# Optimization experiments

Hardware: AMD Instinct MI355X
Metric: run time of the kernel (lower is better)

The kernel has to match this reference:

```python
import jax, jax.numpy as jnp
import numpy as np

INPUT_DIM = 1024
HIDDEN = 64
NUM_MEM = 8   # +1 shared slot -> 9 total
K = 2
SEQ = 256
BATCH = 32


def setup_inputs() -> dict:
    key = jax.random.key(0)
    ks = jax.random.split(key, 10)
    s = 1.0 / np.sqrt(INPUT_DIM)
    nm1 = NUM_MEM + 1
    return {
        "X": jax.random.normal(ks[0], (SEQ, BATCH, INPUT_DIM), jnp.float32),
        "M_0": jnp.zeros((BATCH, nm1, HIDDEN, HIDDEN), jnp.float32),
        "Wk_w": jax.random.uniform(ks[1], (HIDDEN * nm1, INPUT_DIM), jnp.float32, -s, s),
        "Wk_b": jax.random.uniform(ks[2], (HIDDEN * nm1,), jnp.float32, -s, s),
        "Wv_w": jax.random.uniform(ks[3], (HIDDEN * nm1, INPUT_DIM), jnp.float32, -s, s),
        "Wv_b": jax.random.uniform(ks[4], (HIDDEN * nm1,), jnp.float32, -s, s),
        "Wg_w": jax.random.uniform(ks[5], (NUM_MEM, INPUT_DIM), jnp.float32, -s, s),
        "Wg_b": jax.random.uniform(ks[6], (NUM_MEM,), jnp.float32, -s, s),
        "Wq_w": jax.random.uniform(ks[7], (HIDDEN, INPUT_DIM), jnp.float32, -s, s),
        "Wq_b": jax.random.uniform(ks[8], (HIDDEN,), jnp.float32, -s, s),
    }


def _mom_forward(X, M_0, Wk_w, Wk_b, Wv_w, Wv_b, Wg_w, Wg_b, Wq_w, Wq_b):
    B = X.shape[1]
    nm1 = NUM_MEM + 1
    b_idx = jnp.arange(B)[:, None]

    def step(M, x_t):
        # gating + top-k routing (sorted descending, like torch.topk)
        score = jax.nn.softmax(x_t @ Wg_w.T + Wg_b, axis=1)          # (B, NUM_MEM)
        m_scores, m_idx = jax.lax.top_k(score, K)                    # (B, K)
        idx_update = jnp.concatenate(
            [jnp.zeros((B, 1), jnp.int32), m_idx.astype(jnp.int32)], axis=1)  # (B, K+1)
        g = m_scores / jnp.sum(m_scores, axis=1, keepdims=True)     # (B, K)

        Mk = (x_t @ Wk_w.T + Wk_b).reshape(B, nm1, HIDDEN)          # (B, 9, H)
        Mv = (x_t @ Wv_w.T + Wv_b).reshape(B, nm1, HIDDEN)
        # only gather the K+1 routed outer products instead of all 9
        k_sel = jnp.take_along_axis(Mk, idx_update[:, :, None], axis=1)  # (B, K+1, H)
        v_sel = jnp.take_along_axis(Mv, idx_update[:, :, None], axis=1)
        src = k_sel[..., :, None] * v_sel[..., None, :]              # (B, K+1, H, H)
        M = M.at[b_idx, idx_update].add(src)                         # scatter-add (dupes accumulate)

        M_use = M[b_idx, m_idx]                                      # (B, K, H, H)
        M_out = jnp.einsum('bk,bkij->bij', g, M_use) + M[:, 0]       # add shared memory
        q = x_t @ Wq_w.T + Wq_b                                      # (B, H)
        o = jnp.einsum('bi,bij->bj', q, M_out)                       # (B, H)
        return M, o

    M_final, outputs = jax.lax.scan(step, M_0, X)
    return outputs, M_final


def reference(X, M_0, Wk_w, Wk_b, Wv_w, Wv_b, Wg_w, Wg_b, Wq_w, Wq_b):
    return _mom_forward(X, M_0, Wk_w, Wk_b, Wv_w, Wv_b, Wg_w, Wg_b, Wq_w, Wq_b)
```

## Files before the change

### kernel.cpp

```cpp
#include <hip/hip_runtime.h>
#include <stdint.h>

#define SEQ 256
#define BATCH 32
#define IN_DIM 1024
#define HID 64
#define NPAD 1280
#define ROWS (SEQ*BATCH)

#define XBF_OFF   0
#define DMH_OFF   0
#define WBF_OFF   16777216
#define BB_OFF    19398656
#define GATE_OFF  19403776
#define Y_OFF     19534848

#define NC 8
#define CHL 32

#define DM_CB_U32 18432

typedef __attribute__((ext_vector_type(8))) short short8;
typedef __attribute__((ext_vector_type(4))) float floatx4;

typedef const __attribute__((address_space(1))) unsigned int gas_u32;
typedef __attribute__((address_space(3))) unsigned int las_u32;
static __device__ __forceinline__ void gl_lds16(const void* g, void* l) {
  __builtin_amdgcn_global_load_lds((gas_u32*)g, (las_u32*)l, 16, 0, 0);
}

static __device__ __forceinline__ short f2bf(float f) {
  union { float f; uint32_t u; } a; a.f = f;
  uint32_t r = (a.u + 0x7FFFu + ((a.u >> 16) & 1u)) >> 16;
  return (short)r;
}
static __device__ __forceinline__ float bflo(uint32_t u){ return __uint_as_float(u << 16); }
static __device__ __forceinline__ float bfhi(uint32_t u){ return __uint_as_float(u & 0xffff0000u); }
static __device__ __forceinline__ float bfu(unsigned short us){ return __uint_as_float(((uint32_t)us) << 16); }

__global__ __launch_bounds__(256) void prep_gate_kernel(
    const float* __restrict__ X,
    const float* __restrict__ Wk, const float* __restrict__ bk,
    const float* __restrict__ Wv, const float* __restrict__ bv,
    const float* __restrict__ Wg, const float* __restrict__ bg,
    const float* __restrict__ Wq, const float* __restrict__ bq,
    short* __restrict__ Xbf, short* __restrict__ Wbf,
    float* __restrict__ bb, float4* __restrict__ gate)
{
  if (blockIdx.x < 2048) {
    const int lane = threadIdx.x & 63;
    const int row  = blockIdx.x * 4 + (threadIdx.x >> 6);
    const float* x = X + (int64_t)row * IN_DIM;
    short4* xb = (short4*)(Xbf + (int64_t)row * IN_DIM);

    float acc[8];
#pragma unroll
    for (int e = 0; e < 8; e++) acc[e] = 0.f;
#pragma unroll
    for (int i = 0; i < 4; i++) {
      const int off = i * 256 + lane * 4;
      float4 xv = *(const float4*)(x + off);
      short4 s4;
      s4.x = f2bf(xv.x); s4.y = f2bf(xv.y); s4.z = f2bf(xv.z); s4.w = f2bf(xv.w);
      xb[i * 64 + lane] = s4;
#pragma unroll
      for (int e = 0; e < 8; e++) {
        float4 wv = *(const float4*)(Wg + e * IN_DIM + off);
        acc[e] += xv.x * wv.x + xv.y * wv.y + xv.z * wv.z + xv.w * wv.w;
      }
    }
#pragma unroll
    for (int e = 0; e < 8; e++) {
#pragma unroll
      for (int m = 32; m >= 1; m >>= 1)
        acc[e] += __shfl_xor(acc[e], m);
      acc[e] += bg[e];
    }
    if (lane == 0) {
      int i0 = 0; float v0 = acc[0];
#pragma unroll
      for (int e = 1; e < 8; e++) if (acc[e] > v0) { v0 = acc[e]; i0 = e; }
      int i1 = -1; float v1 = -3.4e38f;
#pragma unroll
      for (int e = 0; e < 8; e++) if (e != i0 && acc[e] > v1) { v1 = acc[e]; i1 = e; }
      float e1 = __expf(v1 - v0);
      float inv = 1.f / (1.f + e1);
      gate[row] = make_float4(__int_as_float(i0), __int_as_float(i1), inv, e1 * inv);
    }
  } else {
    const int idx = (blockIdx.x - 2048) * 256 + threadIdx.x;
    const int NW4 = NPAD * IN_DIM / 4;
#pragma unroll
    for (int i = idx; i < NW4; i += 65536) {
      int e = i * 4;
      int r = e >> 10;
      int k = e & 1023;
      float4 x;
      if (r < 576)       x = *(const float4*)(Wk + (int64_t)r*1024 + k);
      else if (r < 1152) x = *(const float4*)(Wv + (int64_t)(r-576)*1024 + k);
      else if (r < 1216) x = *(const float4*)(Wq + (int64_t)(r-1152)*1024 + k);
      else               x = make_float4(0.f, 0.f, 0.f, 0.f);
      short4 s4;
      s4.x = f2bf(x.x); s4.y = f2bf(x.y); s4.z = f2bf(x.z); s4.w = f2bf(x.w);
      ((short4*)Wbf)[i] = s4;
    }
    if (idx < NPAD) {
      int r = idx; float v;
      if (r < 576)       v = bk[r];
      else if (r < 1152) v = bv[r - 576];
      else if (r < 1216) v = bq[r - 1152];
      else               v = 0.f;
      bb[r] = v;
    }
  }
}

__global__ __launch_bounds__(256) void gemm_kernel(
    const short* __restrict__ Xbf,
    const short* __restrict__ Wbf,
    const float* __restrict__ bb,
    float* __restrict__ Y)
{
  __shared__ short As[128 * 32];
  __shared__ short Bs[128 * 32];

  const int tid  = threadIdx.x;
  const int lane = tid & 63;
  const int wv   = tid >> 6;
  const int quad = lane >> 4;
  const int cl   = lane & 15;
  const int wm   = wv & 1;
  const int wn   = wv >> 1;
  const int m0 = blockIdx.y * 128;
  const int n0 = blockIdx.x * 128;

  const int srow = wv * 32 + (lane >> 2);
  const int scol = (lane & 3) * 8;
  const short* gA = Xbf + (int64_t)(m0 + srow) * IN_DIM + scol;
  const short* gB = Wbf + (int64_t)(n0 + srow) * IN_DIM + scol;
  short* lA = As + (wv * 32) * 32;
  short* lB = Bs + (wv * 32) * 32;

  floatx4 acc[4][4];
#pragma unroll
  for (int i = 0; i < 4; i++)
#pragma unroll
    for (int k = 0; k < 4; k++) acc[i][k] = (floatx4){0.f, 0.f, 0.f, 0.f};

  for (int ks = 0; ks < IN_DIM; ks += 32) {
    gl_lds16(gA + ks,                lA);
    gl_lds16(gA + 16 * IN_DIM + ks,  lA + 16 * 32);
    gl_lds16(gB + ks,                lB);
    gl_lds16(gB + 16 * IN_DIM + ks,  lB + 16 * 32);
    __syncthreads();

    short8 bfrag[4], afrag[4];
#pragma unroll
    for (int nt = 0; nt < 4; nt++)
      bfrag[nt] = *(const short8*)(&Bs[(wn * 64 + nt * 16 + cl) * 32 + quad * 8]);
#pragma unroll
    for (int mt = 0; mt < 4; mt++)
      afrag[mt] = *(const short8*)(&As[(wm * 64 + mt * 16 + cl) * 32 + quad * 8]);
#pragma unroll
    for (int mt = 0; mt < 4; mt++)
#pragma unroll
      for (int nt = 0; nt < 4; nt++)
        acc[mt][nt] = __builtin_amdgcn_mfma_f32_16x16x32_bf16(afrag[mt], bfrag[nt], acc[mt][nt], 0, 0, 0);
    __syncthreads();
  }

#pragma unroll
  for (int nt = 0; nt < 4; nt++) {
    const int col = n0 + wn * 64 + nt * 16 + cl;
    const float bias = bb[col];
#pragma unroll
    for (int mt = 0; mt < 4; mt++) {
#pragma unroll
      for (int r = 0; r < 4; r++) {
        int row = m0 + wm * 64 + mt * 16 + quad * 4 + r;
        Y[(int64_t)row * NPAD + col] = acc[mt][nt][r] + bias;
      }
    }
  }
}

__global__ __launch_bounds__(512) void mfma_chunk_kernel(
    const float* __restrict__ Y, const float4* __restrict__ gate,
    unsigned short* __restrict__ DMu, float* __restrict__ out)
{
  __shared__ uint32_t Qs[32 * 32];
  __shared__ uint32_t Ks[96 * 32];
  __shared__ unsigned short Kts[64 * 104];
  __shared__ unsigned short Vts[64 * 104];
  __shared__ unsigned short Ps[32 * 104];
  __shared__ float4 gl[32];
  __shared__ uint32_t su[96];

  const int blk = blockIdx.x;
  const int c   = blk & 7;
  const int b   = blk >> 3;
  const int tid = threadIdx.x;
  const int lane = tid & 63;
  const int wv  = tid >> 6;
  const int quad = lane >> 4;
  const int cl  = lane & 15;
  const int t0  = c * CHL;

  if (tid < 32) {
    float4 g = gate[(t0 + tid) * BATCH + b];
    gl[tid] = g;
    su[3 * tid]     = 0u;
    su[3 * tid + 1] = (uint32_t)__float_as_int(g.x);
    su[3 * tid + 2] = (uint32_t)__float_as_int(g.y);
  }
  __syncthreads();

  for (int idx = tid; idx < 1536; idx += 512) {
    const int e = idx >> 4, d4 = idx & 15;
    const int s = (e * 171) >> 9;
    const int u = e - 3 * s;
    const int head = (u == 0) ? 0 : (int)su[3 * s + u];
    const float* Yr = Y + ((int64_t)(t0 + s) * BATCH + b) * NPAD;
    float4 kf = *(const float4*)(Yr + head * 64 + 4 * d4);
    unsigned short k0 = (unsigned short)f2bf(kf.x), k1 = (unsigned short)f2bf(kf.y);
    unsigned short k2 = (unsigned short)f2bf(kf.z), k3 = (unsigned short)f2bf(kf.w);
    uint2 kp; kp.x = (uint32_t)k0 | ((uint32_t)k1 << 16);
    kp.y = (uint32_t)k2 | ((uint32_t)k3 << 16);
    *(uint2*)&Ks[e * 32 + 2 * d4] = kp;
    Kts[(4 * d4)     * 104 + e] = k0;
    Kts[(4 * d4 + 1) * 104 + e] = k1;
    Kts[(4 * d4 + 2) * 104 + e] = k2;
    Kts[(4 * d4 + 3) * 104 + e] = k3;
    float4 vf = *(const float4*)(Yr + 576 + head * 64 + 4 * d4);
    Vts[(4 * d4)     * 104 + e] = (unsigned short)f2bf(vf.x);
    Vts[(4 * d4 + 1) * 104 + e] = (unsigned short)f2bf(vf.y);
    Vts[(4 * d4 + 2) * 104 + e] = (unsigned short)f2bf(vf.z);
    Vts[(4 * d4 + 3) * 104 + e] = (unsigned short)f2bf(vf.w);
  }
  {
    const int s = tid >> 4, d4 = tid & 15;
    const float* Yr = Y + ((int64_t)(t0 + s) * BATCH + b) * NPAD;
    float4 qf = *(const float4*)(Yr + 1152 + 4 * d4);
    uint2 qp;
    qp.x = (uint32_t)(unsigned short)f2bf(qf.x) | (((uint32_t)(unsigned short)f2bf(qf.y)) << 16);
    qp.y = (uint32_t)(unsigned short)f2bf(qf.z) | (((uint32_t)(unsigned short)f2bf(qf.w)) << 16);
    *(uint2*)&Qs[s * 32 + 2 * d4] = qp;
  }
  __syncthreads();

  const unsigned short* Qu = (const unsigned short*)Qs;
  const unsigned short* Ku = (const unsigned short*)Ks;

  for (int tileId = wv; tileId < 12; tileId += 8) {
    const int mt = tileId / 6, nt = tileId % 6;
    floatx4 acc = (floatx4){0.f, 0.f, 0.f, 0.f};
#pragma unroll
    for (int kc = 0; kc < 2; kc++) {
      short8 af = *(const short8*)(Qu + (mt * 16 + cl) * 64 + kc * 32 + quad * 8);
      short8 bf = *(const short8*)(Ku + (nt * 16 + cl) * 64 + kc * 32 + quad * 8);
      acc = __builtin_amdgcn_mfma_f32_16x16x32_bf16(af, bf, acc, 0, 0, 0);
    }
    const int e = nt * 16 + cl;
    const int s_e = (e * 171) >> 9;
    const int slot_e = (int)su[e];
#pragma unroll
    for (int r = 0; r < 4; r++) {
      const int t = mt * 16 + quad * 4 + r;
      float4 g = gl[t];
      const int i0t = __float_as_int(g.x), i1t = __float_as_int(g.y);
      float w = (slot_e == 0 ? 1.f : 0.f)
              + (slot_e == i0t ? g.z : 0.f)
              + (slot_e == i1t ? g.w : 0.f);
      w = (s_e <= t) ? w : 0.f;
      Ps[t * 104 + e] = (unsigned short)f2bf(w * acc[r]);
    }
  }
  __syncthreads();

  {
    const int tileId = wv;
    const int mt = tileId >> 2, nt = tileId & 3;
    floatx4 acc = (floatx4){0.f, 0.f, 0.f, 0.f};
#pragma unroll
    for (int kc = 0; kc < 3; kc++) {
      short8 af = *(const short8*)(Ps  + (mt * 16 + cl) * 104 + kc * 32 + quad * 8);
      short8 bf = *(const short8*)(Vts + (nt * 16 + cl) * 104 + kc * 32 + quad * 8);
      acc = __builtin_amdgcn_mfma_f32_16x16x32_bf16(af, bf, acc, 0, 0, 0);
    }
#pragma unroll
    for (int r = 0; r < 4; r++) {
      const int t = mt * 16 + quad * 4 + r, j = nt * 16 + cl;
      out[(int64_t)(t0 + t) * (BATCH * HID) + b * HID + j] = acc[r];
    }
  }

  uint32_t sreg[3][8];
#pragma unroll
  for (int kc = 0; kc < 3; kc++)
#pragma unroll
    for (int jj = 0; jj < 8; jj++)
      sreg[kc][jj] = su[kc * 32 + quad * 8 + jj];

  short8 afc[4][3];
#pragma unroll
  for (int mt = 0; mt < 4; mt++)
#pragma unroll
    for (int kc = 0; kc < 3; kc++)
      afc[mt][kc] = *(const short8*)(Kts + (mt * 16 + cl) * 104 + kc * 32 + quad * 8);

  unsigned short* dmb = DMu + ((int64_t)(c * 32 + b)) * 36864;
  union U8 { short8 s; uint32_t u[4]; };

  for (int uu = wv; uu < 36; uu += 8) {
    const int mi = uu >> 2, nt = uu & 3;
    uint32_t md[3][4];
#pragma unroll
    for (int kc = 0; kc < 3; kc++)
#pragma unroll
      for (int p = 0; p < 4; p++)
        md[kc][p] = ((sreg[kc][2 * p]     == (uint32_t)mi) ? 0x0000ffffu : 0u) |
                    ((sreg[kc][2 * p + 1] == (uint32_t)mi) ? 0xffff0000u : 0u);
    short8 bm[3];
#pragma unroll
    for (int kc = 0; kc < 3; kc++) {
      U8 vv; vv.s = *(const short8*)(Vts + (nt * 16 + cl) * 104 + kc * 32 + quad * 8);
      vv.u[0] &= md[kc][0]; vv.u[1] &= md[kc][1];
      vv.u[2] &= md[kc][2]; vv.u[3] &= md[kc][3];
      bm[kc] = vv.s;
    }
#pragma unroll
    for (int mt = 0; mt < 4; mt++) {
      floatx4 acc = (floatx4){0.f, 0.f, 0.f, 0.f};
#pragma unroll
      for (int kc = 0; kc < 3; kc++)
        acc = __builtin_amdgcn_mfma_f32_16x16x32_bf16(afc[mt][kc], bm[kc], acc, 0, 0, 0);
#pragma unroll
      for (int r = 0; r < 4; r++) {
        const int i = mt * 16 + quad * 4 + r, j = nt * 16 + cl;
        dmb[mi * 4096 + i * 64 + j] = (unsigned short)f2bf(acc[r]);
      }
    }
  }
}

__global__ void prefix_kernel(const float* __restrict__ M0, uint32_t* __restrict__ DMh,
                              float* __restrict__ out)
{
  int64_t e = (int64_t)blockIdx.x * blockDim.x + threadIdx.x;
  int b = (int)(e / DM_CB_U32);
  int r = (int)(e % DM_CB_U32);
  int m = r >> 11, rem = r & 2047, i = rem >> 5, jp = rem & 31;
  int64_t f32i = (int64_t)b * 36864 + m * 4096 + i * 64 + jp * 2;
  float run0 = M0[f32i], run1 = M0[f32i + 1];
  uint32_t u[NC];
#pragma unroll
  for (int cc = 0; cc < NC; cc++)
    u[cc] = DMh[((int64_t)(cc * 32 + b)) * DM_CB_U32 + r];
#pragma unroll
  for (int cc = 0; cc < NC; cc++) {
    int64_t idx = ((int64_t)(cc * 32 + b)) * DM_CB_U32 + r;
    DMh[idx] = ((uint32_t)(unsigned short)f2bf(run0)) |
               (((uint32_t)(unsigned short)f2bf(run1)) << 16);
    run0 += bflo(u[cc]); run1 += bfhi(u[cc]);
  }
  *(float2*)(out + (int64_t)SEQ * BATCH * HID + f32i) = make_float2(run0, run1);
}

__global__ __launch_bounds__(256) void corr_kernel(
    const float* __restrict__ Y, const float4* __restrict__ gate,
    const uint32_t* __restrict__ DMh, float* __restrict__ out)
{
  __shared__ unsigned short MsbT[9 * 32 * 68];
  __shared__ float2 qb[32 * 32];
  __shared__ float4 gl[32];
  const int blk = blockIdx.x;
  const int c   = blk & 7;
  const int jh  = (blk >> 3) & 1;
  const int b   = blk >> 4;
  const int tid = threadIdx.x;
  const int t0  = c * CHL;

  if (tid < 32) gl[tid] = gate[(t0 + tid) * BATCH + b];
#pragma unroll
  for (int k = 0; k < 4; k++) {
    int f = tid + 256 * k;
    int t = f >> 5, p = f & 31;
    qb[t * 32 + p] = *(const float2*)(Y + ((int64_t)(t0 + t) * BATCH + b) * NPAD + 1152 + 2 * p);
  }
  const uint32_t* dmb = DMh + ((int64_t)(c * 32 + b)) * DM_CB_U32;
#pragma unroll
  for (int k = 0; k < 36; k++) {
    int f = tid + 256 * k;
    int m = f >> 10, rem = f & 1023, i = rem >> 4, p = rem & 15;
    uint32_t u = dmb[m * 2048 + i * 32 + jh * 16 + p];
    MsbT[(m * 32 + 2 * p)     * 68 + i] = (unsigned short)(u & 0xffffu);
    MsbT[(m * 32 + 2 * p + 1) * 68 + i] = (unsigned short)(u >> 16);
  }
  __syncthreads();

  const int jj = tid & 31;
  const int tg = tid >> 5;
#pragma unroll
  for (int tt = 0; tt < 4; tt++) {
    const int t = tt * 8 + tg;
    float4 g = gl[t];
    const int i0 = __float_as_int(g.x), i1 = __float_as_int(g.y);
    const float g0 = g.z, g1 = g.w;
    const unsigned short* P0 = MsbT + (0  * 32 + jj) * 68;
    const unsigned short* Pa = MsbT + (i0 * 32 + jj) * 68;
    const unsigned short* Pb = MsbT + (i1 * 32 + jj) * 68;
    float acc = 0.f;
#pragma unroll 4
    for (int i4 = 0; i4 < 16; i4++) {
      float2 qq0 = qb[t * 32 + 2 * i4];
      float2 qq1 = qb[t * 32 + 2 * i4 + 1];
      uint2 a0 = *(const uint2*)(P0 + 4 * i4);
      uint2 aa = *(const uint2*)(Pa + 4 * i4);
      uint2 ab = *(const uint2*)(Pb + 4 * i4);
      acc += qq0.x * (bflo(a0.x) + g0 * bflo(aa.x) + g1 * bflo(ab.x));
      acc += qq0.y * (bfhi(a0.x) + g0 * bfhi(aa.x) + g1 * bfhi(ab.x));
      acc += qq1.x * (bflo(a0.y) + g0 * bflo(aa.y) + g1 * bflo(ab.y));
      acc += qq1.y * (bfhi(a0.y) + g0 * bfhi(aa.y) + g1 * bfhi(ab.y));
    }
    float* op = out + (int64_t)(t0 + t) * (BATCH * HID) + b * HID + jh * 32 + jj;
    *op += acc;
  }
}

extern "C" void kernel_launch(void* const* d_in, const int* in_sizes, int n_in,
                              void* d_out, int out_size, void* d_ws, size_t ws_size,
                              hipStream_t stream)
{
  const float* X  = (const float*)d_in[0];
  const float* M0 = (const float*)d_in[1];
  const float* Wk = (const float*)d_in[2];
  const float* bk = (const float*)d_in[3];
  const float* Wv = (const float*)d_in[4];
  const float* bv = (const float*)d_in[5];
  const float* Wg = (const float*)d_in[6];
  const float* bg = (const float*)d_in[7];
  const float* Wq = (const float*)d_in[8];
  const float* bq = (const float*)d_in[9];

  char* ws = (char*)d_ws;
  short*          Xbf  = (short*)(ws + XBF_OFF);
  short*          Wbf  = (short*)(ws + WBF_OFF);
  float*          bb   = (float*)(ws + BB_OFF);
  float4*         gate = (float4*)(ws + GATE_OFF);
  float*          Y    = (float*)(ws + Y_OFF);
  uint32_t*       DMh  = (uint32_t*)(ws + DMH_OFF);
  unsigned short* DMu  = (unsigned short*)(ws + DMH_OFF);
  float*          out  = (float*)d_out;

  prep_gate_kernel<<<2304, 256, 0, stream>>>(X, Wk, bk, Wv, bv, Wg, bg, Wq, bq,
                                             Xbf, Wbf, bb, gate);
  dim3 gg(NPAD / 128, ROWS / 128);
  gemm_kernel<<<gg, 256, 0, stream>>>(Xbf, Wbf, bb, Y);
  mfma_chunk_kernel<<<32 * NC, 512, 0, stream>>>(Y, gate, DMu, out);
  prefix_kernel<<<(32 * DM_CB_U32) / 256, 256, 0, stream>>>(M0, DMh, out);
  corr_kernel<<<32 * NC * 2, 256, 0, stream>>>(Y, gate, DMh, out);
}
```

Measured before the change: 168.2 us.

## Give each wave private double-buffered LDS tiles in GEMM, drop block barriers

The projection GEMM now gives each wave its own private A/B tiles in LDS (64 rows each), double-buffered. Global-to-LDS loads for step k+2 are issued while MFMAs for step k run, with per-wave vmcnt/lgkmcnt waits replacing the block-wide __syncthreads. This removes barrier stalls and overlaps memory latency with compute. The cost is that A and B rows are loaded redundantly across waves (twice the global traffic per block) and LDS use grows to 64KB, which may lower occupancy.

```diff
diff --git a/kernel.cpp b/kernel.cpp
--- a/kernel.cpp
+++ b/kernel.cpp
@@ -121,8 +121,7 @@
     const float* __restrict__ bb,
     float* __restrict__ Y)
 {
-  __shared__ short As[128 * 32];
-  __shared__ short Bs[128 * 32];
+  __shared__ short LDS[4 * 8192];
 
   const int tid  = threadIdx.x;
   const int lane = tid & 63;
@@ -134,12 +133,13 @@
   const int m0 = blockIdx.y * 128;
   const int n0 = blockIdx.x * 128;
 
-  const int srow = wv * 32 + (lane >> 2);
+  short* Abuf = LDS + wv * 8192;
+  short* Bbuf = Abuf + 4096;
+
+  const int srow = lane >> 2;
   const int scol = (lane & 3) * 8;
-  const short* gA = Xbf + (int64_t)(m0 + srow) * IN_DIM + scol;
-  const short* gB = Wbf + (int64_t)(n0 + srow) * IN_DIM + scol;
-  short* lA = As + (wv * 32) * 32;
-  short* lB = Bs + (wv * 32) * 32;
+  const short* gA = Xbf + (int64_t)(m0 + wm * 64 + srow) * IN_DIM + scol;
+  const short* gB = Wbf + (int64_t)(n0 + wn * 64 + srow) * IN_DIM + scol;
 
   floatx4 acc[4][4];
 #pragma unroll
@@ -147,27 +147,67 @@
 #pragma unroll
     for (int k = 0; k < 4; k++) acc[i][k] = (floatx4){0.f, 0.f, 0.f, 0.f};
 
-  for (int ks = 0; ks < IN_DIM; ks += 32) {
-    gl_lds16(gA + ks,                lA);
-    gl_lds16(gA + 16 * IN_DIM + ks,  lA + 16 * 32);
-    gl_lds16(gB + ks,                lB);
-    gl_lds16(gB + 16 * IN_DIM + ks,  lB + 16 * 32);
-    __syncthreads();
-
-    short8 bfrag[4], afrag[4];
-#pragma unroll
-    for (int nt = 0; nt < 4; nt++)
-      bfrag[nt] = *(const short8*)(&Bs[(wn * 64 + nt * 16 + cl) * 32 + quad * 8]);
-#pragma unroll
-    for (int mt = 0; mt < 4; mt++)
-      afrag[mt] = *(const short8*)(&As[(wm * 64 + mt * 16 + cl) * 32 + quad * 8]);
-#pragma unroll
-    for (int mt = 0; mt < 4; mt++)
-#pragma unroll
-      for (int nt = 0; nt < 4; nt++)
-        acc[mt][nt] = __builtin_amdgcn_mfma_f32_16x16x32_bf16(afrag[mt], bfrag[nt], acc[mt][nt], 0, 0, 0);
-    __syncthreads();
-  }
+#define STAGE_AB(BUF, K) do {                          \
+    const short* ga_ = gA + (K) * 32;                  \
+    const short* gb_ = gB + (K) * 32;                  \
+    short* la_ = Abuf + (BUF) * 2048;                  \
+    short* lb_ = Bbuf + (BUF) * 2048;                  \
+    gl_lds16(ga_,                 la_);                \
+    gl_lds16(ga_ + 16 * IN_DIM,   la_ + 512);          \
+    gl_lds16(ga_ + 32 * IN_DIM,   la_ + 1024);         \
+    gl_lds16(ga_ + 48 * IN_DIM,   la_ + 1536);         \
+    gl_lds16(gb_,                 lb_);                \
+    gl_lds16(gb_ + 16 * IN_DIM,   lb_ + 512);          \
+    gl_lds16(gb_ + 32 * IN_DIM,   lb_ + 1024);         \
+    gl_lds16(gb_ + 48 * IN_DIM,   lb_ + 1536);         \
+  } while (0)
+
+  short8 af[4], bf[4];
+#define LOADFRAGS(BUF) do {                                                     \
+    const short* la_ = Abuf + (BUF) * 2048;                                     \
+    const short* lb_ = Bbuf + (BUF) * 2048;                                     \
+    _Pragma("unroll")                                                           \
+    for (int mt = 0; mt < 4; mt++)                                              \
+      af[mt] = *(const short8*)(la_ + (mt * 16 + cl) * 32 + quad * 8);          \
+    _Pragma("unroll")                                                           \
+    for (int nt = 0; nt < 4; nt++)                                              \
+      bf[nt] = *(const short8*)(lb_ + (nt * 16 + cl) * 32 + quad * 8);          \
+  } while (0)
+#define DOMFMA() do {                                                           \
+    _Pragma("unroll")                                                           \
+    for (int mt = 0; mt < 4; mt++)                                              \
+      _Pragma("unroll")                                                         \
+      for (int nt = 0; nt < 4; nt++)                                            \
+        acc[mt][nt] = __builtin_amdgcn_mfma_f32_16x16x32_bf16(af[mt], bf[nt], acc[mt][nt], 0, 0, 0); \
+  } while (0)
+
+  STAGE_AB(0, 0);
+  STAGE_AB(1, 1);
+
+#pragma unroll 2
+  for (int k = 0; k < 30; k++) {
+    const int cur = k & 1;
+    asm volatile("s_waitcnt vmcnt(8)" ::: "memory");
+    __builtin_amdgcn_sched_barrier(0);
+    LOADFRAGS(cur);
+    asm volatile("s_waitcnt lgkmcnt(0)" ::: "memory");
+    __builtin_amdgcn_sched_barrier(0);
+    STAGE_AB(cur, k + 2);
+    __builtin_amdgcn_sched_barrier(0);
+    DOMFMA();
+  }
+  asm volatile("s_waitcnt vmcnt(8)" ::: "memory");
+  __builtin_amdgcn_sched_barrier(0);
+  LOADFRAGS(0);
+  DOMFMA();
+  asm volatile("s_waitcnt vmcnt(0)" ::: "memory");
+  __builtin_amdgcn_sched_barrier(0);
+  LOADFRAGS(1);
+  DOMFMA();
+
+#undef STAGE_AB
+#undef LOADFRAGS
+#undef DOMFMA
 
 #pragma unroll
   for (int nt = 0; nt < 4; nt++) {
```

New measurement: 182.5 us. +8.5%, slower.
